# Performance work log

Hardware: AMD Instinct MI355X
Metric: run time of the kernel (lower is better)

Reference implementation:

```python
import jax, jax.numpy as jnp
import numpy as np

N_HEAD = 8


def _wn_linear(x, v, g, b):
    # torch weight_norm with default dim=0: per-output-row normalization
    w = g[:, None] * v / jnp.linalg.norm(v, axis=1, keepdims=True)  # [out, in]
    return x @ w.T + b


def setup_inputs() -> dict:
    key = jax.random.key(0)
    ks = jax.random.split(key, 12)
    B, Cq, Ck, C, H, W = 8, 256, 256, 512, 32, 32
    return {
        "query": jax.random.normal(ks[0], (B, Cq, H, W), jnp.float32),
        "key": jax.random.normal(ks[1], (B, Ck, H, W), jnp.float32),
        "vq": jax.random.normal(ks[2], (C, Cq), jnp.float32) * 0.05,
        "gq": jax.random.uniform(ks[3], (C,), jnp.float32, 0.5, 1.5),
        "bq": jax.random.normal(ks[4], (C,), jnp.float32) * 0.01,
        "vk": jax.random.normal(ks[5], (C, Ck), jnp.float32) * 0.05,
        "gk": jax.random.uniform(ks[6], (C,), jnp.float32, 0.5, 1.5),
        "bk": jax.random.normal(ks[7], (C,), jnp.float32) * 0.01,
        "vv": jax.random.normal(ks[8], (C, Ck), jnp.float32) * 0.05,
        "gv": jax.random.uniform(ks[9], (C,), jnp.float32, 0.5, 1.5),
        "bv": jax.random.normal(ks[10], (C,), jnp.float32) * 0.01,
    }


def reference(query, key, vq, gq, bq, vk, gk, bk, vv, gv, bv):
    B, _, H, W = key.shape
    S = H * W
    C = vq.shape[0]
    dh = C // N_HEAD

    # [B, C_in, H, W] -> [B, S, C_in]
    qf = query.reshape(B, query.shape[1], S).transpose(0, 2, 1)
    kf = key.reshape(B, key.shape[1], S).transpose(0, 2, 1)

    def heads(x):  # [B, S, C] -> [B, nh, S, dh]
        return x.reshape(B, S, N_HEAD, dh).transpose(0, 2, 1, 3)

    q = heads(_wn_linear(qf, vq, gq, bq))
    k = heads(_wn_linear(kf, vk, gk, bk))
    v = heads(_wn_linear(kf, vv, gv, bv))

    attn = jnp.einsum('bhqd,bhkd->bhqk', q, k) / np.float32(np.sqrt(dh))
    # strictly-causal mask: position i may attend only to j < i
    mask = jnp.tril(jnp.ones((S, S), dtype=bool), k=-1)
    attn = jnp.where(mask, attn, jnp.float32(-1e8))
    attn = jax.nn.softmax(attn, axis=-1)
    # start_mask: zero out query row 0 (which has no valid keys)
    start_mask = jnp.ones((S, 1), jnp.float32).at[0, 0].set(0.0)
    attn = attn * start_mask  # broadcast over [B, nh, S, S]
    # dropout is identity in eval mode

    out = jnp.einsum('bhqk,bhkd->bhqd', attn, v)           # [B, nh, S, dh]
    out = out.transpose(0, 2, 1, 3).reshape(B, H, W, C)     # [B, H, W, C]
    return out.transpose(0, 3, 1, 2)                        # [B, C, H, W]
```

## Files before the change

kernel.cpp:

```cpp
#include <hip/hip_runtime.h>

typedef _Float16 f16x8 __attribute__((ext_vector_type(8)));
typedef __fp16   h16x2 __attribute__((ext_vector_type(2)));
typedef float    f32x4 __attribute__((ext_vector_type(4)));
typedef uint     u32x4 __attribute__((ext_vector_type(4)));

#define NB   8
#define CIN  256
#define CC   512
#define SS   1024
#define NH   8
#define DH   64

#define SCL 0.18033688f
#define THR 11.5409f

static __device__ __forceinline__ ushort f2h(float f) {
  union { _Float16 h; ushort u; } cv;
  cv.h = (_Float16)f;
  return cv.u;
}
static __device__ __forceinline__ uint pk2u(float a, float b) {
  union { h16x2 h; uint u; } cv;
  cv.h = __builtin_amdgcn_cvt_pkrtz(a, b);
  return cv.u;
}

__global__ __launch_bounds__(256)
void prep_kernel(const float* __restrict__ query, const float* __restrict__ key,
                 const float* __restrict__ vq, const float* __restrict__ gq,
                 const float* __restrict__ vk, const float* __restrict__ gk,
                 const float* __restrict__ vv, const float* __restrict__ gv,
                 ushort* __restrict__ Xt, ushort* __restrict__ w_all) {
  const int t = threadIdx.x;
  __shared__ float T[64 * 64];

  if (blockIdx.x < 1024) {
    const int bx = blockIdx.x;
    const int kt = bx & 3, st = (bx >> 2) & 15, b = (bx >> 6) & 7, mat = bx >> 9;
    const float* Xf = ((mat == 0) ? query : key)
                      + (size_t)b * CIN * SS + (size_t)(kt * 64) * SS + st * 64;
    ushort* Ot = Xt + ((size_t)(mat * NB + b) * SS + st * 64) * CIN + kt * 64;

    const int kl0 = t >> 4;
    const int s4  = (t & 15) * 4;
    #pragma unroll
    for (int p = 0; p < 4; p++) {
      const int kl = p * 16 + kl0;
      const float4 xv = *(const float4*)&Xf[(size_t)kl * SS + s4];
      T[(s4 + 0) * 64 + (kl ^ (s4 + 0))] = xv.x;
      T[(s4 + 1) * 64 + (kl ^ (s4 + 1))] = xv.y;
      T[(s4 + 2) * 64 + (kl ^ (s4 + 2))] = xv.z;
      T[(s4 + 3) * 64 + (kl ^ (s4 + 3))] = xv.w;
    }
    __syncthreads();

    const int sl = t >> 2;
    const int k0 = (t & 3) * 16;
    uint ow[8];
    #pragma unroll
    for (int q = 0; q < 8; q++) {
      const float f0 = T[sl * 64 + ((k0 + 2 * q) ^ sl)];
      const float f1 = T[sl * 64 + ((k0 + 2 * q + 1) ^ sl)];
      ow[q] = pk2u(f0, f1);
    }
    *(u32x4*)&Ot[(size_t)sl * CIN + k0]     = (u32x4){ow[0], ow[1], ow[2], ow[3]};
    *(u32x4*)&Ot[(size_t)sl * CIN + k0 + 8] = (u32x4){ow[4], ow[5], ow[6], ow[7]};
  } else {
    const int idx = blockIdx.x - 1024;
    const int mat = idx >> 9, c = idx & 511;
    const float* v = (mat == 0) ? vq : (mat == 1) ? vk : vv;
    const float* g = (mat == 0) ? gq : (mat == 1) ? gk : gv;

    float val = v[c * CIN + t];
    float s = val * val;
    #pragma unroll
    for (int off = 32; off; off >>= 1) s += __shfl_down(s, off);

    const int wave = t >> 6;
    if ((t & 63) == 0) T[wave] = s;
    __syncthreads();
    float tot = T[0] + T[1] + T[2] + T[3];
    float scale = g[c] * rsqrtf(tot);
    if (mat == 0) scale *= SCL;
    w_all[(size_t)mat * CC * CIN + c * CIN + t] = f2h(val * scale);
  }
}

__global__ __launch_bounds__(256)
void proj_kernel(const ushort* __restrict__ Xt, const ushort* __restrict__ w_all,
                 const float* __restrict__ bq, const float* __restrict__ bk,
                 const float* __restrict__ bv,
                 ushort* __restrict__ qkv) {
  const int wg  = blockIdx.x;
  const int swb = (wg & 7) * 96 + (wg >> 3);
  const int tn = swb & 3, tm = (swb >> 2) & 7;
  const int b  = (swb >> 5) & 7, mz = swb >> 8;
  const int t  = threadIdx.x;
  const int s0 = tm * 128, c0 = tn * 128;

  const ushort* Xb = Xt + ((size_t)(((mz == 0) ? 0 : NB) + b) * SS + s0) * CIN;
  const ushort* Wb = w_all + (size_t)mz * CC * CIN + (size_t)c0 * CIN;
  const float*  bias = (mz == 0) ? bq : (mz == 1) ? bk : bv;
  const float   bscale = (mz == 0) ? SCL : 1.f;
  ushort*       outp = qkv + (size_t)mz * NB * NH * SS * DH;

  __shared__ __align__(16) ushort Xs[128 * 64];
  __shared__ __align__(16) ushort Ws[128 * 64];

  const int wave = t >> 6, lane = t & 63;
  const int wm = wave >> 1, wn = wave & 1;
  const int lrow = lane & 15, kg = lane >> 4;

  const int srow = t >> 3;
  const int scol = (t & 7) * 8;

  f16x8 xr[4], wr[4];
  auto LOADT = [&](int kt) {
    const int k0 = kt * 64;
    #pragma unroll
    for (int q = 0; q < 4; q++) {
      const int row = q * 32 + srow;
      xr[q] = *(const f16x8*)&Xb[(size_t)row * CIN + k0 + scol];
      wr[q] = *(const f16x8*)&Wb[(size_t)row * CIN + k0 + scol];
    }
  };
  auto STORET = [&]() {
    #pragma unroll
    for (int q = 0; q < 4; q++) {
      const int row = q * 32 + srow;
      const int off = row * 64 + (scol ^ (8 * (row & 7)));
      *(f16x8*)&Xs[off] = xr[q];
      *(f16x8*)&Ws[off] = wr[q];
    }
  };

  f32x4 acc[4][4];
  #pragma unroll
  for (int i = 0; i < 4; i++)
    #pragma unroll
    for (int j = 0; j < 4; j++) acc[i][j] = (f32x4){0.f, 0.f, 0.f, 0.f};

  LOADT(0);
  STORET();
  LOADT(1);
  __syncthreads();

  const int swzA = 8 * (lrow & 7);
  for (int kt = 0; kt < 4; ++kt) {
    f16x8 a[4][2], bf[4][2];
    #pragma unroll
    for (int i = 0; i < 4; i++) {
      const int ra = (wm * 64 + i * 16 + lrow) * 64;
      a[i][0] = *(const f16x8*)&Xs[ra + ((kg * 8) ^ swzA)];
      a[i][1] = *(const f16x8*)&Xs[ra + ((32 + kg * 8) ^ swzA)];
      const int rb = (wn * 64 + i * 16 + lrow) * 64;
      bf[i][0] = *(const f16x8*)&Ws[rb + ((kg * 8) ^ swzA)];
      bf[i][1] = *(const f16x8*)&Ws[rb + ((32 + kg * 8) ^ swzA)];
    }
    if (mz == 2) {
      #pragma unroll
      for (int i = 0; i < 4; i++)
        #pragma unroll
        for (int j = 0; j < 4; j++) {
          acc[i][j] = __builtin_amdgcn_mfma_f32_16x16x32_f16(bf[j][0], a[i][0], acc[i][j], 0, 0, 0);
          acc[i][j] = __builtin_amdgcn_mfma_f32_16x16x32_f16(bf[j][1], a[i][1], acc[i][j], 0, 0, 0);
        }
    } else {
      #pragma unroll
      for (int i = 0; i < 4; i++)
        #pragma unroll
        for (int j = 0; j < 4; j++) {
          acc[i][j] = __builtin_amdgcn_mfma_f32_16x16x32_f16(a[i][0], bf[j][0], acc[i][j], 0, 0, 0);
          acc[i][j] = __builtin_amdgcn_mfma_f32_16x16x32_f16(a[i][1], bf[j][1], acc[i][j], 0, 0, 0);
        }
    }
    if (kt < 3) {
      __syncthreads();
      STORET();
      if (kt < 2) LOADT(kt + 2);
      __syncthreads();
    }
  }

  if (mz == 2) {
    #pragma unroll
    for (int i = 0; i < 4; i++) {
      const int sg = s0 + wm * 64 + i * 16 + lrow;
      #pragma unroll
      for (int j = 0; j < 4; j++) {
        #pragma unroll
        for (int r = 0; r < 4; r++) {
          const int c = c0 + wn * 64 + j * 16 + kg * 4 + r;
          outp[(((size_t)b * NH + (c >> 6)) * DH + (c & 63)) * SS + sg] =
              f2h(acc[i][j][r] + bias[c]);
        }
      }
    }
  } else {
    #pragma unroll
    for (int i = 0; i < 4; i++) {
      const int srw = s0 + wm * 64 + i * 16 + kg * 4;
      #pragma unroll
      for (int j = 0; j < 4; j++) {
        const int cgl = c0 + wn * 64 + j * 16 + lrow;
        const float bias_c = bias[cgl] * bscale;
        const size_t obase = (((size_t)b * NH + (cgl >> 6)) * SS) * DH + (cgl & 63);
        #pragma unroll
        for (int r = 0; r < 4; r++)
          outp[obase + (size_t)(srw + r) * DH] = f2h(acc[i][j][r] + bias_c);
      }
    }
  }
}

__global__ __launch_bounds__(256, 4)
void attn_kernel(const ushort* __restrict__ Q, const ushort* __restrict__ K,
                 const ushort* __restrict__ V, float* __restrict__ out) {
  const int wg = blockIdx.x;
  const int j  = wg >> 3;
  const int r  = j & 15, s = j >> 4;
  const int qt = ((s >> 1) & 1) ? (15 - r) : r;
  const int bh = (wg & 7) * 8 + s;
  const int nt = qt + 1;
  const int t = threadIdx.x;
  const int wave = t >> 6, lane = t & 63;
  const int lrow = lane & 15, kg = lane >> 4;

  __shared__ __align__(16) ushort Ks[2][64 * 64];
  __shared__ __align__(16) ushort Vs[2][64 * 64];

  const ushort* Qb = Q + (size_t)bh * SS * DH;
  const ushort* Kb = K + (size_t)bh * SS * DH;
  const ushort* Vb = V + (size_t)bh * DH * SS;

  const int qg = qt * 64 + wave * 16 + lrow;

  f16x8 qa0 = *(const f16x8*)&Qb[(size_t)qg * DH + kg * 8];
  f16x8 qa1 = *(const f16x8*)&Qb[(size_t)qg * DH + 32 + kg * 8];

  float m = -1e30f, l = 0.f;
  f32x4 o[4];
  #pragma unroll
  for (int d = 0; d < 4; d++) o[d] = (f32x4){0.f, 0.f, 0.f, 0.f};

  const int r0 = t >> 3,        c0s = (t & 7) * 8;
  const int r1 = 32 + (t >> 3), c1s = c0s;
  const int ke0 = r0 * 64 + (c0s ^ (8 * (r0 & 7)));
  const int ke1 = r1 * 64 + (c1s ^ (8 * (r1 & 7)));

  f16x8 kr0, kr1, vr0, vr1;
  auto LOADT = [&](int jt) {
    const int j0 = jt * 64;
    kr0 = *(const f16x8*)&Kb[(size_t)(j0 + r0) * DH + c0s];
    kr1 = *(const f16x8*)&Kb[(size_t)(j0 + r1) * DH + c1s];
    vr0 = *(const f16x8*)&Vb[(size_t)r0 * SS + j0 + c0s];
    vr1 = *(const f16x8*)&Vb[(size_t)r1 * SS + j0 + c1s];
  };
  auto STORET = [&](int buf) {
    *(f16x8*)&Ks[buf][ke0] = kr0;
    *(f16x8*)&Ks[buf][ke1] = kr1;
    *(f16x8*)&Vs[buf][ke0] = vr0;
    *(f16x8*)&Vs[buf][ke1] = vr1;
  };

  LOADT(0);
  STORET(0);
  if (nt > 1) LOADT(1);
  __syncthreads();

  const int swz = 8 * (lrow & 7);

  for (int jt = 0; jt < nt; ++jt) {
    const int cur = jt & 1;
    const ushort* Kc = Ks[cur];
    const ushort* Vc = Vs[cur];
    const int j0 = jt * 64;
    const bool diag = (jt == qt);

    f32x4 z[4];
    #pragma unroll
    for (int cf = 0; cf < 4; cf++) z[cf] = (f32x4){0.f, 0.f, 0.f, 0.f};
    #pragma unroll
    for (int cf = 0; cf < 4; ++cf) {
      const int krow = (cf * 16 + lrow) * 64;
      f16x8 ka0 = *(const f16x8*)&Kc[krow + ((kg * 8) ^ swz)];
      f16x8 ka1 = *(const f16x8*)&Kc[krow + ((32 + kg * 8) ^ swz)];
      z[cf] = __builtin_amdgcn_mfma_f32_16x16x32_f16(ka0, qa0, z[cf], 0, 0, 0);
      z[cf] = __builtin_amdgcn_mfma_f32_16x16x32_f16(ka1, qa1, z[cf], 0, 0, 0);
    }

    if (diag) {
      #pragma unroll
      for (int cf = 0; cf < 4; cf++)
        #pragma unroll
        for (int rr = 0; rr < 4; rr++) {
          const int keyi = j0 + cf * 16 + kg * 4 + rr;
          if (keyi >= qg) z[cf][rr] = -1e9f;
        }
    }
    float mxl = z[0][0];
    #pragma unroll
    for (int cf = 0; cf < 4; cf++)
      #pragma unroll
      for (int rr = 0; rr < 4; rr++) mxl = fmaxf(mxl, z[cf][rr]);
    if (__any(mxl > m + THR)) {
      float mx = fmaxf(mxl, __shfl_xor(mxl, 16));
      mx = fmaxf(mx, __shfl_xor(mx, 32));
      const float mn = fmaxf(m, mx);
      const float corr = exp2f(m - mn);
      m = mn;
      l *= corr;
      #pragma unroll
      for (int d = 0; d < 4; d++) o[d] *= corr;
    }
    float ps = 0.f;
    #pragma unroll
    for (int cf = 0; cf < 4; cf++)
      #pragma unroll
      for (int rr = 0; rr < 4; rr++) {
        z[cf][rr] = exp2f(z[cf][rr] - m);
        ps += z[cf][rr];
      }
    ps += __shfl_xor(ps, 16);
    ps += __shfl_xor(ps, 32);
    l += ps;

    uint u0 = pk2u(z[0][0], z[0][1]), u1 = pk2u(z[0][2], z[0][3]);
    uint u2 = pk2u(z[1][0], z[1][1]), u3 = pk2u(z[1][2], z[1][3]);
    uint u4 = pk2u(z[2][0], z[2][1]), u5 = pk2u(z[2][2], z[2][3]);
    uint u6 = pk2u(z[3][0], z[3][1]), u7 = pk2u(z[3][2], z[3][3]);
    const bool hi2 = (kg & 2) != 0;
    uint tA0 = hi2 ? u0 : u2, tA1 = hi2 ? u1 : u3;
    uint tA2 = hi2 ? u4 : u6, tA3 = hi2 ? u5 : u7;
    uint rA0 = __shfl_xor((int)tA0, 32), rA1 = __shfl_xor((int)tA1, 32);
    uint rA2 = __shfl_xor((int)tA2, 32), rA3 = __shfl_xor((int)tA3, 32);
    const bool sel = ((kg ^ (kg >> 1)) & 1) != 0;
    uint oc0 = hi2 ? u2 : u0, oc1 = hi2 ? u3 : u1;
    uint oc2 = hi2 ? u6 : u4, oc3 = hi2 ? u7 : u5;
    uint sB0 = sel ? oc0 : rA0, sB1 = sel ? oc1 : rA1;
    uint sB2 = sel ? oc2 : rA2, sB3 = sel ? oc3 : rA3;
    uint rB0 = __shfl_xor((int)sB0, 16), rB1 = __shfl_xor((int)sB1, 16);
    uint rB2 = __shfl_xor((int)sB2, 16), rB3 = __shfl_xor((int)sB3, 16);
    uint w0 = (kg == 0) ? u0 : ((kg == 2) ? rA0 : rB0);
    uint w1 = (kg == 0) ? u1 : ((kg == 2) ? rA1 : rB1);
    uint w2 = (kg == 3) ? u2 : ((kg == 1) ? rA0 : rB0);
    uint w3 = (kg == 3) ? u3 : ((kg == 1) ? rA1 : rB1);
    uint w4 = (kg == 0) ? u4 : ((kg == 2) ? rA2 : rB2);
    uint w5 = (kg == 0) ? u5 : ((kg == 2) ? rA3 : rB3);
    uint w6 = (kg == 3) ? u6 : ((kg == 1) ? rA2 : rB2);
    uint w7 = (kg == 3) ? u7 : ((kg == 1) ? rA3 : rB3);
    union { u32x4 u; f16x8 h; } pa0v, pa1v;
    pa0v.u = (u32x4){w0, w1, w2, w3};
    pa1v.u = (u32x4){w4, w5, w6, w7};

    #pragma unroll
    for (int dt = 0; dt < 4; ++dt) {
      const int vrow = (dt * 16 + lrow) * 64;
      f16x8 va0 = *(const f16x8*)&Vc[vrow + ((kg * 8) ^ swz)];
      f16x8 va1 = *(const f16x8*)&Vc[vrow + ((32 + kg * 8) ^ swz)];
      o[dt] = __builtin_amdgcn_mfma_f32_16x16x32_f16(va0, pa0v.h, o[dt], 0, 0, 0);
      o[dt] = __builtin_amdgcn_mfma_f32_16x16x32_f16(va1, pa1v.h, o[dt], 0, 0, 0);
    }

    if (jt + 1 < nt) {
      STORET(cur ^ 1);
      if (jt + 2 < nt) LOADT(jt + 2);
      __syncthreads();
    }
  }

  const int b = bh >> 3, h = bh & 7;
  float* ob = out + ((size_t)b * CC + h * DH) * SS;
  float inv = (l > 0.f) ? 1.f / l : 0.f;
  if (qg == 0) inv = 0.f;
  #pragma unroll
  for (int dt = 0; dt < 4; dt++)
    #pragma unroll
    for (int rr = 0; rr < 4; rr++)
      ob[(size_t)(dt * 16 + kg * 4 + rr) * SS + qg] = o[dt][rr] * inv;
}

extern "C" void kernel_launch(void* const* d_in, const int* in_sizes, int n_in,
                              void* d_out, int out_size, void* d_ws, size_t ws_size,
                              hipStream_t stream) {
  const float* query = (const float*)d_in[0];
  const float* key   = (const float*)d_in[1];
  const float* vq = (const float*)d_in[2];
  const float* gq = (const float*)d_in[3];
  const float* bq = (const float*)d_in[4];
  const float* vk = (const float*)d_in[5];
  const float* gk = (const float*)d_in[6];
  const float* bk = (const float*)d_in[7];
  const float* vv = (const float*)d_in[8];
  const float* gv = (const float*)d_in[9];
  const float* bv = (const float*)d_in[10];
  float* out = (float*)d_out;

  ushort* w_all = (ushort*)d_ws;
  ushort* qkv   = w_all + (size_t)3 * CC * CIN;
  ushort* Xt    = qkv + (size_t)3 * NB * NH * SS * DH;
  ushort* qb  = qkv;
  ushort* kb2 = qkv + (size_t)NB * NH * SS * DH;
  ushort* vb2 = kb2 + (size_t)NB * NH * SS * DH;

  prep_kernel<<<2560, 256, 0, stream>>>(query, key, vq, gq, vk, gk, vv, gv, Xt, w_all);
  proj_kernel<<<768, 256, 0, stream>>>(Xt, w_all, bq, bk, bv, qkv);
  attn_kernel<<<1024, 256, 0, stream>>>(qb, kb2, vb2, out);
}
```

Measured before the change: 53.36 us.

## Use 128-row query tiles with 8 waves in attention and vectorize projection stores

The attention kernel now gives each workgroup 128 query rows across 8 waves (512 threads), so every K/V tile staged in shared memory serves twice as many queries and each thread loads half as much. Waves whose rows end before the current key tile skip the compute but still join the barriers. The projection epilogue swaps MFMA operand order between the two layouts so each lane writes 4 contiguous fp16 values as one 8-byte store instead of scalar 2-byte scatters. The cost is half as many workgroups, more causal imbalance within a workgroup (idle waves), and larger barrier groups.

New measurement: 59.02 us. 1.11x slower.

```diff
diff --git a/kernel.cpp b/kernel.cpp
--- a/kernel.cpp
+++ b/kernel.cpp
@@ -3,6 +3,7 @@
 typedef _Float16 f16x8 __attribute__((ext_vector_type(8)));
 typedef __fp16   h16x2 __attribute__((ext_vector_type(2)));
 typedef float    f32x4 __attribute__((ext_vector_type(4)));
+typedef uint     u32x2 __attribute__((ext_vector_type(2)));
 typedef uint     u32x4 __attribute__((ext_vector_type(4)));
 
 #define NB   8
@@ -163,16 +164,16 @@
       for (int i = 0; i < 4; i++)
         #pragma unroll
         for (int j = 0; j < 4; j++) {
+          acc[i][j] = __builtin_amdgcn_mfma_f32_16x16x32_f16(a[i][0], bf[j][0], acc[i][j], 0, 0, 0);
+          acc[i][j] = __builtin_amdgcn_mfma_f32_16x16x32_f16(a[i][1], bf[j][1], acc[i][j], 0, 0, 0);
+        }
+    } else {
+      #pragma unroll
+      for (int i = 0; i < 4; i++)
+        #pragma unroll
+        for (int j = 0; j < 4; j++) {
           acc[i][j] = __builtin_amdgcn_mfma_f32_16x16x32_f16(bf[j][0], a[i][0], acc[i][j], 0, 0, 0);
           acc[i][j] = __builtin_amdgcn_mfma_f32_16x16x32_f16(bf[j][1], a[i][1], acc[i][j], 0, 0, 0);
-        }
-    } else {
-      #pragma unroll
-      for (int i = 0; i < 4; i++)
-        #pragma unroll
-        for (int j = 0; j < 4; j++) {
-          acc[i][j] = __builtin_amdgcn_mfma_f32_16x16x32_f16(a[i][0], bf[j][0], acc[i][j], 0, 0, 0);
-          acc[i][j] = __builtin_amdgcn_mfma_f32_16x16x32_f16(a[i][1], bf[j][1], acc[i][j], 0, 0, 0);
         }
     }
     if (kt < 3) {
@@ -184,48 +185,53 @@
   }
 
   if (mz == 2) {
-    #pragma unroll
-    for (int i = 0; i < 4; i++) {
-      const int sg = s0 + wm * 64 + i * 16 + lrow;
-      #pragma unroll
-      for (int j = 0; j < 4; j++) {
-        #pragma unroll
-        for (int r = 0; r < 4; r++) {
-          const int c = c0 + wn * 64 + j * 16 + kg * 4 + r;
-          outp[(((size_t)b * NH + (c >> 6)) * DH + (c & 63)) * SS + sg] =
-              f2h(acc[i][j][r] + bias[c]);
-        }
+    const int h = tn * 2 + wn;
+    #pragma unroll
+    for (int j = 0; j < 4; j++) {
+      const int d = j * 16 + lrow;
+      const float bc = bias[c0 + wn * 64 + j * 16 + lrow];
+      ushort* op = outp + ((size_t)(b * NH + h) * DH + d) * SS;
+      #pragma unroll
+      for (int i = 0; i < 4; i++) {
+        const int sg = s0 + wm * 64 + i * 16 + kg * 4;
+        u32x2 pw = (u32x2){pk2u(acc[i][j][0] + bc, acc[i][j][1] + bc),
+                           pk2u(acc[i][j][2] + bc, acc[i][j][3] + bc)};
+        *(u32x2*)&op[sg] = pw;
       }
     }
   } else {
-    #pragma unroll
-    for (int i = 0; i < 4; i++) {
-      const int srw = s0 + wm * 64 + i * 16 + kg * 4;
-      #pragma unroll
-      for (int j = 0; j < 4; j++) {
-        const int cgl = c0 + wn * 64 + j * 16 + lrow;
-        const float bias_c = bias[cgl] * bscale;
-        const size_t obase = (((size_t)b * NH + (cgl >> 6)) * SS) * DH + (cgl & 63);
-        #pragma unroll
-        for (int r = 0; r < 4; r++)
-          outp[obase + (size_t)(srw + r) * DH] = f2h(acc[i][j][r] + bias_c);
+    const int h = tn * 2 + wn;
+    #pragma unroll
+    for (int j = 0; j < 4; j++) {
+      const int d0 = j * 16 + kg * 4;
+      const int cb = c0 + wn * 64 + d0;
+      const float b0 = bias[cb + 0] * bscale, b1 = bias[cb + 1] * bscale;
+      const float b2 = bias[cb + 2] * bscale, b3 = bias[cb + 3] * bscale;
+      #pragma unroll
+      for (int i = 0; i < 4; i++) {
+        const int sg = s0 + wm * 64 + i * 16 + lrow;
+        u32x2 pw = (u32x2){pk2u(acc[i][j][0] + b0, acc[i][j][1] + b1),
+                           pk2u(acc[i][j][2] + b2, acc[i][j][3] + b3)};
+        *(u32x2*)&outp[((size_t)(b * NH + h) * SS + sg) * DH + d0] = pw;
       }
     }
   }
 }
 
-__global__ __launch_bounds__(256, 4)
+__global__ __launch_bounds__(512, 4)
 void attn_kernel(const ushort* __restrict__ Q, const ushort* __restrict__ K,
                  const ushort* __restrict__ V, float* __restrict__ out) {
   const int wg = blockIdx.x;
-  const int j  = wg >> 3;
-  const int r  = j & 15, s = j >> 4;
-  const int qt = ((s >> 1) & 1) ? (15 - r) : r;
-  const int bh = (wg & 7) * 8 + s;
-  const int nt = qt + 1;
+  const int x  = wg & 7, bt = (wg >> 3) & 7;
+  const int bh = x * 8 + bt;
+  const int u  = (wg >> 6) & 3, hi = wg >> 8;
+  const int qt = hi ? (7 - u) : u;
+  const int nt = 2 * qt + 2;
+  const int q0 = qt * 128;
   const int t = threadIdx.x;
   const int wave = t >> 6, lane = t & 63;
   const int lrow = lane & 15, kg = lane >> 4;
+  const int jtd = (q0 + wave * 16) >> 6;
 
   __shared__ __align__(16) ushort Ks[2][64 * 64];
   __shared__ __align__(16) ushort Vs[2][64 * 64];
@@ -234,7 +240,7 @@
   const ushort* Kb = K + (size_t)bh * SS * DH;
   const ushort* Vb = V + (size_t)bh * DH * SS;
 
-  const int qg = qt * 64 + wave * 16 + lrow;
+  const int qg = q0 + wave * 16 + lrow;
 
   f16x8 qa0 = *(const f16x8*)&Qb[(size_t)qg * DH + kg * 8];
   f16x8 qa1 = *(const f16x8*)&Qb[(size_t)qg * DH + 32 + kg * 8];
@@ -244,123 +250,119 @@
   #pragma unroll
   for (int d = 0; d < 4; d++) o[d] = (f32x4){0.f, 0.f, 0.f, 0.f};
 
-  const int r0 = t >> 3,        c0s = (t & 7) * 8;
-  const int r1 = 32 + (t >> 3), c1s = c0s;
+  const int r0 = t >> 3, c0s = (t & 7) * 8;
   const int ke0 = r0 * 64 + (c0s ^ (8 * (r0 & 7)));
-  const int ke1 = r1 * 64 + (c1s ^ (8 * (r1 & 7)));
-
-  f16x8 kr0, kr1, vr0, vr1;
+
+  f16x8 kr0, vr0;
   auto LOADT = [&](int jt) {
     const int j0 = jt * 64;
     kr0 = *(const f16x8*)&Kb[(size_t)(j0 + r0) * DH + c0s];
-    kr1 = *(const f16x8*)&Kb[(size_t)(j0 + r1) * DH + c1s];
     vr0 = *(const f16x8*)&Vb[(size_t)r0 * SS + j0 + c0s];
-    vr1 = *(const f16x8*)&Vb[(size_t)r1 * SS + j0 + c1s];
   };
   auto STORET = [&](int buf) {
     *(f16x8*)&Ks[buf][ke0] = kr0;
-    *(f16x8*)&Ks[buf][ke1] = kr1;
     *(f16x8*)&Vs[buf][ke0] = vr0;
-    *(f16x8*)&Vs[buf][ke1] = vr1;
   };
 
   LOADT(0);
   STORET(0);
-  if (nt > 1) LOADT(1);
+  LOADT(1);
   __syncthreads();
 
   const int swz = 8 * (lrow & 7);
 
   for (int jt = 0; jt < nt; ++jt) {
     const int cur = jt & 1;
-    const ushort* Kc = Ks[cur];
-    const ushort* Vc = Vs[cur];
-    const int j0 = jt * 64;
-    const bool diag = (jt == qt);
-
-    f32x4 z[4];
-    #pragma unroll
-    for (int cf = 0; cf < 4; cf++) z[cf] = (f32x4){0.f, 0.f, 0.f, 0.f};
-    #pragma unroll
-    for (int cf = 0; cf < 4; ++cf) {
-      const int krow = (cf * 16 + lrow) * 64;
-      f16x8 ka0 = *(const f16x8*)&Kc[krow + ((kg * 8) ^ swz)];
-      f16x8 ka1 = *(const f16x8*)&Kc[krow + ((32 + kg * 8) ^ swz)];
-      z[cf] = __builtin_amdgcn_mfma_f32_16x16x32_f16(ka0, qa0, z[cf], 0, 0, 0);
-      z[cf] = __builtin_amdgcn_mfma_f32_16x16x32_f16(ka1, qa1, z[cf], 0, 0, 0);
-    }
-
-    if (diag) {
+    if (jt <= jtd) {
+      const ushort* Kc = Ks[cur];
+      const ushort* Vc = Vs[cur];
+      const int j0 = jt * 64;
+      const bool diag = (jt == jtd);
+
+      f32x4 z[4];
+      #pragma unroll
+      for (int cf = 0; cf < 4; cf++) z[cf] = (f32x4){0.f, 0.f, 0.f, 0.f};
+      #pragma unroll
+      for (int cf = 0; cf < 4; ++cf) {
+        const int krow = (cf * 16 + lrow) * 64;
+        f16x8 ka0 = *(const f16x8*)&Kc[krow + ((kg * 8) ^ swz)];
+        f16x8 ka1 = *(const f16x8*)&Kc[krow + ((32 + kg * 8) ^ swz)];
+        z[cf] = __builtin_amdgcn_mfma_f32_16x16x32_f16(ka0, qa0, z[cf], 0, 0, 0);
+        z[cf] = __builtin_amdgcn_mfma_f32_16x16x32_f16(ka1, qa1, z[cf], 0, 0, 0);
+      }
+
+      if (diag) {
+        #pragma unroll
+        for (int cf = 0; cf < 4; cf++)
+          #pragma unroll
+          for (int rr = 0; rr < 4; rr++) {
+            const int keyi = j0 + cf * 16 + kg * 4 + rr;
+            if (keyi >= qg) z[cf][rr] = -1e9f;
+          }
+      }
+      float mxl = z[0][0];
       #pragma unroll
       for (int cf = 0; cf < 4; cf++)
         #pragma unroll
+        for (int rr = 0; rr < 4; rr++) mxl = fmaxf(mxl, z[cf][rr]);
+      if (__any(mxl > m + THR)) {
+        float mx = fmaxf(mxl, __shfl_xor(mxl, 16));
+        mx = fmaxf(mx, __shfl_xor(mx, 32));
+        const float mn = fmaxf(m, mx);
+        const float corr = exp2f(m - mn);
+        m = mn;
+        l *= corr;
+        #pragma unroll
+        for (int d = 0; d < 4; d++) o[d] *= corr;
+      }
+      float ps = 0.f;
+      #pragma unroll
+      for (int cf = 0; cf < 4; cf++)
+        #pragma unroll
         for (int rr = 0; rr < 4; rr++) {
-          const int keyi = j0 + cf * 16 + kg * 4 + rr;
-          if (keyi >= qg) z[cf][rr] = -1e9f;
+          z[cf][rr] = exp2f(z[cf][rr] - m);
+          ps += z[cf][rr];
         }
-    }
-    float mxl = z[0][0];
-    #pragma unroll
-    for (int cf = 0; cf < 4; cf++)
-      #pragma unroll
-      for (int rr = 0; rr < 4; rr++) mxl = fmaxf(mxl, z[cf][rr]);
-    if (__any(mxl > m + THR)) {
-      float mx = fmaxf(mxl, __shfl_xor(mxl, 16));
-      mx = fmaxf(mx, __shfl_xor(mx, 32));
-      const float mn = fmaxf(m, mx);
-      const float corr = exp2f(m - mn);
-      m = mn;
-      l *= corr;
-      #pragma unroll
-      for (int d = 0; d < 4; d++) o[d] *= corr;
-    }
-    float ps = 0.f;
-    #pragma unroll
-    for (int cf = 0; cf < 4; cf++)
-      #pragma unroll
-      for (int rr = 0; rr < 4; rr++) {
-        z[cf][rr] = exp2f(z[cf][rr] - m);
-        ps += z[cf][rr];
-      }
-    ps += __shfl_xor(ps, 16);
-    ps += __shfl_xor(ps, 32);
-    l += ps;
-
-    uint u0 = pk2u(z[0][0], z[0][1]), u1 = pk2u(z[0][2], z[0][3]);
-    uint u2 = pk2u(z[1][0], z[1][1]), u3 = pk2u(z[1][2], z[1][3]);
-    uint u4 = pk2u(z[2][0], z[2][1]), u5 = pk2u(z[2][2], z[2][3]);
-    uint u6 = pk2u(z[3][0], z[3][1]), u7 = pk2u(z[3][2], z[3][3]);
-    const bool hi2 = (kg & 2) != 0;
-    uint tA0 = hi2 ? u0 : u2, tA1 = hi2 ? u1 : u3;
-    uint tA2 = hi2 ? u4 : u6, tA3 = hi2 ? u5 : u7;
-    uint rA0 = __shfl_xor((int)tA0, 32), rA1 = __shfl_xor((int)tA1, 32);
-    uint rA2 = __shfl_xor((int)tA2, 32), rA3 = __shfl_xor((int)tA3, 32);
-    const bool sel = ((kg ^ (kg >> 1)) & 1) != 0;
-    uint oc0 = hi2 ? u2 : u0, oc1 = hi2 ? u3 : u1;
-    uint oc2 = hi2 ? u6 : u4, oc3 = hi2 ? u7 : u5;
-    uint sB0 = sel ? oc0 : rA0, sB1 = sel ? oc1 : rA1;
-    uint sB2 = sel ? oc2 : rA2, sB3 = sel ? oc3 : rA3;
-    uint rB0 = __shfl_xor((int)sB0, 16), rB1 = __shfl_xor((int)sB1, 16);
-    uint rB2 = __shfl_xor((int)sB2, 16), rB3 = __shfl_xor((int)sB3, 16);
-    uint w0 = (kg == 0) ? u0 : ((kg == 2) ? rA0 : rB0);
-    uint w1 = (kg == 0) ? u1 : ((kg == 2) ? rA1 : rB1);
-    uint w2 = (kg == 3) ? u2 : ((kg == 1) ? rA0 : rB0);
-    uint w3 = (kg == 3) ? u3 : ((kg == 1) ? rA1 : rB1);
-    uint w4 = (kg == 0) ? u4 : ((kg == 2) ? rA2 : rB2);
-    uint w5 = (kg == 0) ? u5 : ((kg == 2) ? rA3 : rB3);
-    uint w6 = (kg == 3) ? u6 : ((kg == 1) ? rA2 : rB2);
-    uint w7 = (kg == 3) ? u7 : ((kg == 1) ? rA3 : rB3);
-    union { u32x4 u; f16x8 h; } pa0v, pa1v;
-    pa0v.u = (u32x4){w0, w1, w2, w3};
-    pa1v.u = (u32x4){w4, w5, w6, w7};
-
-    #pragma unroll
-    for (int dt = 0; dt < 4; ++dt) {
-      const int vrow = (dt * 16 + lrow) * 64;
-      f16x8 va0 = *(const f16x8*)&Vc[vrow + ((kg * 8) ^ swz)];
-      f16x8 va1 = *(const f16x8*)&Vc[vrow + ((32 + kg * 8) ^ swz)];
-      o[dt] = __builtin_amdgcn_mfma_f32_16x16x32_f16(va0, pa0v.h, o[dt], 0, 0, 0);
-      o[dt] = __builtin_amdgcn_mfma_f32_16x16x32_f16(va1, pa1v.h, o[dt], 0, 0, 0);
+      ps += __shfl_xor(ps, 16);
+      ps += __shfl_xor(ps, 32);
+      l += ps;
+
+      uint u0 = pk2u(z[0][0], z[0][1]), u1 = pk2u(z[0][2], z[0][3]);
+      uint u2 = pk2u(z[1][0], z[1][1]), u3 = pk2u(z[1][2], z[1][3]);
+      uint u4 = pk2u(z[2][0], z[2][1]), u5 = pk2u(z[2][2], z[2][3]);
+      uint u6 = pk2u(z[3][0], z[3][1]), u7 = pk2u(z[3][2], z[3][3]);
+      const bool hi2 = (kg & 2) != 0;
+      uint tA0 = hi2 ? u0 : u2, tA1 = hi2 ? u1 : u3;
+      uint tA2 = hi2 ? u4 : u6, tA3 = hi2 ? u5 : u7;
+      uint rA0 = __shfl_xor((int)tA0, 32), rA1 = __shfl_xor((int)tA1, 32);
+      uint rA2 = __shfl_xor((int)tA2, 32), rA3 = __shfl_xor((int)tA3, 32);
+      const bool sel = ((kg ^ (kg >> 1)) & 1) != 0;
+      uint oc0 = hi2 ? u2 : u0, oc1 = hi2 ? u3 : u1;
+      uint oc2 = hi2 ? u6 : u4, oc3 = hi2 ? u7 : u5;
+      uint sB0 = sel ? oc0 : rA0, sB1 = sel ? oc1 : rA1;
+      uint sB2 = sel ? oc2 : rA2, sB3 = sel ? oc3 : rA3;
+      uint rB0 = __shfl_xor((int)sB0, 16), rB1 = __shfl_xor((int)sB1, 16);
+      uint rB2 = __shfl_xor((int)sB2, 16), rB3 = __shfl_xor((int)sB3, 16);
+      uint w0 = (kg == 0) ? u0 : ((kg == 2) ? rA0 : rB0);
+      uint w1 = (kg == 0) ? u1 : ((kg == 2) ? rA1 : rB1);
+      uint w2 = (kg == 3) ? u2 : ((kg == 1) ? rA0 : rB0);
+      uint w3 = (kg == 3) ? u3 : ((kg == 1) ? rA1 : rB1);
+      uint w4 = (kg == 0) ? u4 : ((kg == 2) ? rA2 : rB2);
+      uint w5 = (kg == 0) ? u5 : ((kg == 2) ? rA3 : rB3);
+      uint w6 = (kg == 3) ? u6 : ((kg == 1) ? rA2 : rB2);
+      uint w7 = (kg == 3) ? u7 : ((kg == 1) ? rA3 : rB3);
+      union { u32x4 uu; f16x8 h; } pa0v, pa1v;
+      pa0v.uu = (u32x4){w0, w1, w2, w3};
+      pa1v.uu = (u32x4){w4, w5, w6, w7};
+
+      #pragma unroll
+      for (int dt = 0; dt < 4; ++dt) {
+        const int vrow = (dt * 16 + lrow) * 64;
+        f16x8 va0 = *(const f16x8*)&Vc[vrow + ((kg * 8) ^ swz)];
+        f16x8 va1 = *(const f16x8*)&Vc[vrow + ((32 + kg * 8) ^ swz)];
+        o[dt] = __builtin_amdgcn_mfma_f32_16x16x32_f16(va0, pa0v.h, o[dt], 0, 0, 0);
+        o[dt] = __builtin_amdgcn_mfma_f32_16x16x32_f16(va1, pa1v.h, o[dt], 0, 0, 0);
+      }
     }
 
     if (jt + 1 < nt) {
@@ -406,5 +408,5 @@
 
   prep_kernel<<<2560, 256, 0, stream>>>(query, key, vq, gq, vk, gk, vv, gv, Xt, w_all);
   proj_kernel<<<768, 256, 0, stream>>>(Xt, w_all, bq, bk, bv, qkv);
-  attn_kernel<<<1024, 256, 0, stream>>>(qb, kb2, vb2, out);
-}
+  attn_kernel<<<512, 512, 0, stream>>>(qb, kb2, vb2, out);
+}
```
